# Optimization experiments

Hardware: AMD Instinct MI355X
Metric: run time of the kernel (lower is better)

The kernel has to match this reference:

```python
import jax, jax.numpy as jnp
import numpy as np


def setup_inputs() -> dict:
    key = jax.random.key(0)
    kx, kw = jax.random.split(key)
    B, C, O, H, W = 16, 32, 32, 256, 256
    x = jax.random.normal(kx, (B, C, H, W), dtype=jnp.float32)
    # Xavier-uniform init for weights of shape (O, C, H, W):
    fan_in = C * H * W
    fan_out = O * H * W
    limit = float(np.sqrt(6.0 / (fan_in + fan_out)))
    weights = jax.random.uniform(kw, (O, C, H, W), dtype=jnp.float32,
                                 minval=-limit, maxval=limit)
    return {"x": x, "weights": weights}


def reference(x, weights):
    # x: (B, C, H, W) real; weights: (O, C, H, W) real
    B, C, H, W = x.shape
    x_f = jnp.fft.rfft2(x)        # (B, C, H, W//2+1) complex
    k_f = jnp.fft.rfft2(weights)  # (O, C, H, W//2+1) complex
    # Contract channels per frequency bin instead of materializing
    # the B x O x C x H x (W//2+1) broadcast intermediate.
    out_f = jnp.einsum("bchw,ochw->bohw", x_f, k_f)
    out = jnp.fft.irfft2(out_f, s=(H, W))  # (B, O, H, W) real
    return out
```

## Files before the change

### kernel.cpp

```cpp
#include <hip/hip_runtime.h>
#include <math.h>


#define PITCH 136
#define SW(i) ((i) + ((i) >> 4))

__device__ __forceinline__ int drev4(int x) {
  int r = (int)(__brev((unsigned)x) >> 24);
  return ((r & 0x55) << 1) | ((r >> 1) & 0x55);
}

__device__ __forceinline__ void fill_tw256(float2* tw, float sign, int tid) {
  float ang = sign * 6.2831853071795864769f * (float)tid * (1.0f / 256.0f);
  float s, c;
  __sincosf(ang, &s, &c);
  tw[tid] = make_float2(c, s);
}

__device__ __forceinline__ float2 cmul(float2 a, float2 b) {
  return make_float2(fmaf(a.x, b.x, -(a.y * b.y)), fmaf(a.x, b.y, a.y * b.x));
}

template <int SIGN>
__device__ __forceinline__ void bfly4(float2 x0, float2 x1, float2 x2, float2 x3,
                                      float2 t1, float2 t2, float2 t3,
                                      float2& y0, float2& y1, float2& y2, float2& y3) {
  float2 a1 = cmul(x1, t1);
  float2 a2 = cmul(x2, t2);
  float2 a3 = cmul(x3, t3);
  float Ax = x0.x + a2.x, Ay = x0.y + a2.y;
  float Bx = x0.x - a2.x, By = x0.y - a2.y;
  float Cx = a1.x + a3.x, Cy = a1.y + a3.y;
  float Dx = a1.x - a3.x, Dy = a1.y - a3.y;
  y0 = make_float2(Ax + Cx, Ay + Cy);
  y2 = make_float2(Ax - Cx, Ay - Cy);
  if (SIGN == 1) {
    y1 = make_float2(Bx - Dy, By + Dx);
    y3 = make_float2(Bx + Dy, By - Dx);
  } else {
    y1 = make_float2(Bx + Dy, By - Dx);
    y3 = make_float2(Bx - Dy, By + Dx);
  }
}

__global__ __launch_bounds__(256) void rfft_rows(const float* __restrict__ xin,
                                                 const float* __restrict__ win,
                                                 float2* __restrict__ xout,
                                                 float2* __restrict__ wout) {
  __shared__ float2 sc[4 * 272];
  __shared__ float2 tw[256];
  const int tid = threadIdx.x;
  fill_tw256(tw, -1.f, tid);
  int blk = blockIdx.x;
  const float* in;
  float2* out;
  if (blk < 16384) {
    in = xin + (long)blk * 8 * 256;
    out = xout + (long)blk * 8 * PITCH;
  } else {
    blk -= 16384;
    in = win + (long)blk * 8 * 256;
    out = wout + (long)blk * 8 * PITCH;
  }
  const int p = tid >> 6, lt = tid & 63;
  float2* s = sc + p * 272;
  {
    int n0 = lt * 4;
    float4 v0 = *(const float4*)(in + (2 * p) * 256 + n0);
    float4 v1 = *(const float4*)(in + (2 * p + 1) * 256 + n0);
    s[SW(drev4(n0))]     = make_float2(v0.x, v1.x);
    s[SW(drev4(n0 + 1))] = make_float2(v0.y, v1.y);
    s[SW(drev4(n0 + 2))] = make_float2(v0.z, v1.z);
    s[SW(drev4(n0 + 3))] = make_float2(v0.w, v1.w);
  }
  __syncthreads();
#pragma unroll
  for (int st = 0; st < 4; ++st) {
    const int sh2 = 2 * st;
    const int L = 1 << sh2;
    const int sh = 6 - sh2;
    int j = lt & (L - 1);
    int i0 = ((lt >> sh2) << (sh2 + 2)) + j;
    float2 t1 = tw[j << sh];
    float2 t2 = tw[(2 * j) << sh];
    float2 t3 = tw[(3 * j) << sh];
    float2 x0 = s[SW(i0)], x1 = s[SW(i0 + L)];
    float2 x2 = s[SW(i0 + 2 * L)], x3 = s[SW(i0 + 3 * L)];
    float2 y0, y1, y2, y3;
    bfly4<-1>(x0, x1, x2, x3, t1, t2, t3, y0, y1, y2, y3);
    s[SW(i0)] = y0;
    s[SW(i0 + L)] = y1;
    s[SW(i0 + 2 * L)] = y2;
    s[SW(i0 + 3 * L)] = y3;
    __syncthreads();
  }
  float2* op0 = out + (2 * p) * PITCH;
  float2* op1 = out + (2 * p + 1) * PITCH;
#pragma unroll
  for (int half = 0; half < 2; ++half) {
    int k = lt + 64 * half;
    float2 U = s[SW(k)];
    float2 Vc = s[SW((256 - k) & 255)];
    float2 V = make_float2(Vc.x, -Vc.y);
    float2 A = make_float2(0.5f * (U.x + V.x), 0.5f * (U.y + V.y));
    float Wx = U.x - V.x, Wy = U.y - V.y;
    float2 Bv = make_float2(0.5f * Wy, -0.5f * Wx);
    op0[k] = A;
    op1[k] = Bv;
  }
  if (lt == 0) {
    float2 Z = s[SW(128)];
    op0[128] = make_float2(Z.x, 0.f);
    op1[128] = make_float2(Z.y, 0.f);
  }
}

template <int SIGN, int TW_>
__device__ __forceinline__ void fft_cols_body(float2* __restrict__ base,
                                              float2* __restrict__ sc,
                                              const float2* __restrict__ tw,
                                              int tid) {
  constexpr int LGT = (TW_ == 16) ? 4 : 3;
#pragma unroll
  for (int r = 0; r < TW_ / 2; ++r) {
    int f = r * 256 + tid;
    int c2 = f & (TW_ / 2 - 1);
    int h = f >> (LGT - 1);
    float4 v = *(const float4*)(base + (long)h * PITCH + c2 * 2);
    int hb = drev4(h);
    sc[hb * TW_ + c2 * 2]     = make_float2(v.x, v.y);
    sc[hb * TW_ + c2 * 2 + 1] = make_float2(v.z, v.w);
  }
  __syncthreads();
#pragma unroll
  for (int st = 0; st < 4; ++st) {
    const int sh2 = 2 * st;
    const int L = 1 << sh2;
    const int sh = 6 - sh2;
#pragma unroll
    for (int q = 0; q < TW_ / 4; ++q) {
      int e = q * 256 + tid;
      int col = e & (TW_ - 1);
      int k = e >> LGT;
      int j = k & (L - 1);
      int i0 = ((k >> sh2) << (sh2 + 2)) + j;
      float2 t1 = tw[j << sh];
      float2 t2 = tw[(2 * j) << sh];
      float2 t3 = tw[(3 * j) << sh];
      float2* p0 = &sc[i0 * TW_ + col];
      float2 x0 = p0[0], x1 = p0[L * TW_], x2 = p0[2 * L * TW_], x3 = p0[3 * L * TW_];
      float2 y0, y1, y2, y3;
      bfly4<SIGN>(x0, x1, x2, x3, t1, t2, t3, y0, y1, y2, y3);
      p0[0] = y0;
      p0[L * TW_] = y1;
      p0[2 * L * TW_] = y2;
      p0[3 * L * TW_] = y3;
    }
    __syncthreads();
  }
#pragma unroll
  for (int r = 0; r < TW_ / 2; ++r) {
    int f = r * 256 + tid;
    int c2 = f & (TW_ / 2 - 1);
    int h = f >> (LGT - 1);
    float2 a = sc[h * TW_ + c2 * 2], b = sc[h * TW_ + c2 * 2 + 1];
    *(float4*)(base + (long)h * PITCH + c2 * 2) = make_float4(a.x, a.y, b.x, b.y);
  }
}

template <int SIGN>
__global__ __launch_bounds__(256) void fft_cols(float2* __restrict__ data) {
  __shared__ float2 sc[256 * 16];
  __shared__ float2 tw[256];
  const int tid = threadIdx.x;
  fill_tw256(tw, (float)SIGN, tid);
  if (blockIdx.y < 8) {
    float2* base = data + (long)blockIdx.x * 256 * PITCH + blockIdx.y * 16;
    fft_cols_body<SIGN, 16>(base, sc, tw, tid);
  } else {
    float2* base = data + (long)blockIdx.x * 256 * PITCH + 128;
    fft_cols_body<SIGN, 8>(base, sc, tw, tid);
  }
}

__global__ __launch_bounds__(256, 3) void einsum_kernel(float2* __restrict__ xf,
                                                        const float2* __restrict__ wf) {
  __shared__ __align__(16) float2 Xs[8 * 256];
  __shared__ __align__(16) float2 Ws[8 * 32 * 16];
  const int h = blockIdx.x;
  const int tid = threadIdx.x;

  if (blockIdx.y == 8) {
    const long off = (long)h * PITCH + 128;
    for (int e = tid; e < 512; e += 256)  Xs[e] = xf[(long)e * 256 * PITCH + off];
    for (int e = tid; e < 1024; e += 256) Ws[e] = wf[(long)e * 256 * PITCH + off];
    __syncthreads();
    const int b = tid >> 4, o0 = (tid & 15) * 2;
    float2 a0 = make_float2(0.f, 0.f), a1 = make_float2(0.f, 0.f);
#pragma unroll
    for (int c = 0; c < 32; ++c) {
      float2 x = Xs[b * 32 + c];
      float2 w0 = Ws[o0 * 32 + c];
      float2 w1 = Ws[(o0 + 1) * 32 + c];
      a0.x = fmaf(x.x, w0.x, fmaf(-x.y, w0.y, a0.x));
      a0.y = fmaf(x.x, w0.y, fmaf(x.y, w0.x, a0.y));
      a1.x = fmaf(x.x, w1.x, fmaf(-x.y, w1.y, a1.x));
      a1.y = fmaf(x.x, w1.y, fmaf(x.y, w1.x, a1.y));
    }
    xf[(long)(b * 32 + o0) * 256 * PITCH + off] = a0;
    xf[(long)(b * 32 + o0 + 1) * 256 * PITCH + off] = a1;
    return;
  }

  const int wb = tid & 15, b = tid >> 4;
  const long hoff = (long)h * PITCH + blockIdx.y * 16;
  float2 acc[32];
#pragma unroll
  for (int o = 0; o < 32; ++o) acc[o] = make_float2(0.f, 0.f);

  const float2* gX[4];
  float2* sX[4];
#pragma unroll
  for (int r = 0; r < 4; ++r) {
    int e = r * 256 + tid, lw = e & 7, lc = (e >> 3) & 7, lb = e >> 6;
    gX[r] = xf + (long)(lb * 32 + lc) * 256 * PITCH + hoff + lw * 2;
    sX[r] = &Xs[lc * 256 + lb * 16 + lw * 2];
  }
  const float2* gW[8];
  float2* sW[8];
#pragma unroll
  for (int r = 0; r < 8; ++r) {
    int e = r * 256 + tid, lw = e & 7, lc = (e >> 3) & 7, lo = e >> 6;
    gW[r] = wf + (long)(lo * 32 + lc) * 256 * PITCH + hoff + lw * 2;
    sW[r] = &Ws[(lc * 32 + lo) * 16 + lw * 2];
  }
  const long cstep = (long)8 * 256 * PITCH;

  float4 px[4], pw[8];
#pragma unroll
  for (int r = 0; r < 4; ++r) px[r] = *(const float4*)gX[r];
#pragma unroll
  for (int r = 0; r < 8; ++r) pw[r] = *(const float4*)gW[r];

  for (int c0 = 0; c0 < 32; c0 += 8) {
#pragma unroll
    for (int r = 0; r < 4; ++r) *(float4*)sX[r] = px[r];
#pragma unroll
    for (int r = 0; r < 8; ++r) *(float4*)sW[r] = pw[r];
    __syncthreads();
    if (c0 < 24) {
#pragma unroll
      for (int r = 0; r < 4; ++r) { gX[r] += cstep; px[r] = *(const float4*)gX[r]; }
#pragma unroll
      for (int r = 0; r < 8; ++r) { gW[r] += cstep; pw[r] = *(const float4*)gW[r]; }
    }
#pragma unroll
    for (int c = 0; c < 8; ++c) {
      float2 xv = Xs[c * 256 + tid];
#pragma unroll
      for (int o = 0; o < 32; ++o) {
        float2 wv = Ws[(c * 32 + o) * 16 + wb];
        acc[o].x = fmaf(xv.x, wv.x, fmaf(-xv.y, wv.y, acc[o].x));
        acc[o].y = fmaf(xv.x, wv.y, fmaf(xv.y, wv.x, acc[o].y));
      }
    }
    __syncthreads();
  }
#pragma unroll
  for (int o = 0; o < 32; ++o)
    xf[(long)(b * 32 + o) * 256 * PITCH + hoff + wb] = acc[o];
}

__global__ __launch_bounds__(256) void irfft_rows(const float2* __restrict__ in,
                                                  float* __restrict__ out) {
  __shared__ float2 sc[4 * 272];
  __shared__ float2 tw[256];
  const int tid = threadIdx.x;
  fill_tw256(tw, 1.f, tid);
  const long row0 = (long)blockIdx.x * 8;
  const int p = tid >> 6, lt = tid & 63;
  float2* s = sc + p * 272;
  const float2* ip0 = in + (row0 + 2 * p) * PITCH;
  const float2* ip1 = in + (row0 + 2 * p + 1) * PITCH;
#pragma unroll
  for (int q = 0; q < 4; ++q) {
    int k = lt + 64 * q;
    int m = (k <= 128) ? k : 256 - k;
    float2 U0 = ip0[m], U1 = ip1[m];
    float2 z;
    if (k <= 128) z = make_float2(U0.x - U1.y, U0.y + U1.x);
    else          z = make_float2(U0.x + U1.y, U1.x - U0.y);
    s[SW(drev4(k))] = z;
  }
  __syncthreads();
#pragma unroll
  for (int st = 0; st < 4; ++st) {
    const int sh2 = 2 * st;
    const int L = 1 << sh2;
    const int sh = 6 - sh2;
    int j = lt & (L - 1);
    int i0 = ((lt >> sh2) << (sh2 + 2)) + j;
    float2 t1 = tw[j << sh];
    float2 t2 = tw[(2 * j) << sh];
    float2 t3 = tw[(3 * j) << sh];
    float2 x0 = s[SW(i0)], x1 = s[SW(i0 + L)];
    float2 x2 = s[SW(i0 + 2 * L)], x3 = s[SW(i0 + 3 * L)];
    float2 y0, y1, y2, y3;
    bfly4<1>(x0, x1, x2, x3, t1, t2, t3, y0, y1, y2, y3);
    s[SW(i0)] = y0;
    s[SW(i0 + L)] = y1;
    s[SW(i0 + 2 * L)] = y2;
    s[SW(i0 + 3 * L)] = y3;
    __syncthreads();
  }
  const float scale = 1.f / 65536.f;
  float* o0 = out + (row0 + 2 * p) * 256;
  float* o1 = out + (row0 + 2 * p + 1) * 256;
  int n0 = lt * 4;
  float2 e0 = s[SW(n0)], e1 = s[SW(n0 + 1)], e2 = s[SW(n0 + 2)], e3 = s[SW(n0 + 3)];
  *(float4*)(o0 + n0) = make_float4(e0.x * scale, e1.x * scale, e2.x * scale, e3.x * scale);
  *(float4*)(o1 + n0) = make_float4(e0.y * scale, e1.y * scale, e2.y * scale, e3.y * scale);
}

extern "C" void kernel_launch(void* const* d_in, const int* in_sizes, int n_in,
                              void* d_out, int out_size, void* d_ws, size_t ws_size,
                              hipStream_t stream) {
  const float* x = (const float*)d_in[0];
  const float* w = (const float*)d_in[1];
  float* out = (float*)d_out;

  const size_t row_elems = (size_t)256 * PITCH;
  const size_t need = (size_t)(512 + 1024) * row_elems * sizeof(float2);
  if (ws_size < need) return;

  float2* Xf = (float2*)d_ws;
  float2* Wf = Xf + (size_t)512 * row_elems;

  rfft_rows<<<dim3(16384 + 32768), 256, 0, stream>>>(x, w, Xf, Wf);
  fft_cols<-1><<<dim3(1536, 9), 256, 0, stream>>>(Xf);
  einsum_kernel<<<dim3(256, 9), 256, 0, stream>>>(Xf, Wf);
  fft_cols<1><<<dim3(512, 9), 256, 0, stream>>>(Xf);
  irfft_rows<<<dim3(16384), 256, 0, stream>>>(Xf, out);
}
```

Baseline: 1.085 ms.

## Use register radix-16 four-step FFT for column transforms; drop einsum register prefetch

Column FFTs on 16-wide tiles switch from four shared-memory radix-4 stages with a barrier after each to a 16x16 four-step decomposition done in registers: a DFT16, a twiddle multiply, a transpose through shared memory, and a second DFT16. This removes the bit-reversal load and most of the shared-memory round trips and barriers. The einsum kernel separately drops its register double-buffered global prefetch in favour of direct load-then-store into shared memory, which frees registers but exposes load latency. A barrier is added after the twiddle table fill.

```diff
diff --git a/kernel.cpp b/kernel.cpp
--- a/kernel.cpp
+++ b/kernel.cpp
@@ -43,6 +43,33 @@
   }
 }
 
+template <int SIGN>
+__device__ __forceinline__ void dft16(float2 v[16]) {
+  const float C1 = 0.92387953251128675613f;
+  const float S1 = 0.38268343236508977173f;
+  const float R2 = 0.70710678118654752440f;
+  const float s = (float)SIGN;
+  const float2 ONE = make_float2(1.f, 0.f);
+  const float2 W1 = make_float2(C1, s * S1);
+  const float2 W2 = make_float2(R2, s * R2);
+  const float2 W3 = make_float2(S1, s * C1);
+  const float2 W4 = make_float2(0.f, s);
+  const float2 W6 = make_float2(-R2, s * R2);
+  const float2 W9 = make_float2(-C1, -s * S1);
+  float2 t[4][4];
+#pragma unroll
+  for (int b = 0; b < 4; ++b)
+    bfly4<SIGN>(v[b], v[b + 4], v[b + 8], v[b + 12], ONE, ONE, ONE,
+                t[b][0], t[b][1], t[b][2], t[b][3]);
+  t[1][1] = cmul(t[1][1], W1); t[1][2] = cmul(t[1][2], W2); t[1][3] = cmul(t[1][3], W3);
+  t[2][1] = cmul(t[2][1], W2); t[2][2] = cmul(t[2][2], W4); t[2][3] = cmul(t[2][3], W6);
+  t[3][1] = cmul(t[3][1], W3); t[3][2] = cmul(t[3][2], W6); t[3][3] = cmul(t[3][3], W9);
+#pragma unroll
+  for (int k1 = 0; k1 < 4; ++k1)
+    bfly4<SIGN>(t[0][k1], t[1][k1], t[2][k1], t[3][k1], ONE, ONE, ONE,
+                v[k1], v[k1 + 4], v[k1 + 8], v[k1 + 12]);
+}
+
 __global__ __launch_bounds__(256) void rfft_rows(const float* __restrict__ xin,
                                                  const float* __restrict__ win,
                                                  float2* __restrict__ xout,
@@ -115,12 +142,56 @@
   }
 }
 
-template <int SIGN, int TW_>
-__device__ __forceinline__ void fft_cols_body(float2* __restrict__ base,
-                                              float2* __restrict__ sc,
-                                              const float2* __restrict__ tw,
-                                              int tid) {
-  constexpr int LGT = (TW_ == 16) ? 4 : 3;
+template <int SIGN>
+__device__ __forceinline__ void fft_cols_body16(float2* __restrict__ base,
+                                                float2* __restrict__ sc,
+                                                const float2* __restrict__ tw,
+                                                int tid) {
+#pragma unroll
+  for (int r = 0; r < 8; ++r) {
+    int f = r * 256 + tid;
+    int c2 = f & 7;
+    int h = f >> 3;
+    float4 v = *(const float4*)(base + (long)h * PITCH + c2 * 2);
+    sc[h * 16 + c2 * 2]     = make_float2(v.x, v.y);
+    sc[h * 16 + c2 * 2 + 1] = make_float2(v.z, v.w);
+  }
+  __syncthreads();
+  const int wb = tid & 15, n1 = tid >> 4;
+  float2 xr[16];
+#pragma unroll
+  for (int n2 = 0; n2 < 16; ++n2) xr[n2] = sc[(16 * n2 + n1) * 16 + wb];
+  dft16<SIGN>(xr);
+#pragma unroll
+  for (int K = 1; K < 16; ++K) xr[K] = cmul(xr[K], tw[n1 * K]);
+  __syncthreads();
+#pragma unroll
+  for (int K = 0; K < 16; ++K) sc[(n1 * 16 + K) * 16 + wb] = xr[K];
+  __syncthreads();
+  const int k1 = tid >> 4;
+  float2 zr[16];
+#pragma unroll
+  for (int m = 0; m < 16; ++m) zr[m] = sc[(m * 16 + k1) * 16 + wb];
+  dft16<SIGN>(zr);
+#pragma unroll
+  for (int k2 = 0; k2 < 16; ++k2) sc[(k1 + 16 * k2) * 16 + wb] = zr[k2];
+  __syncthreads();
+#pragma unroll
+  for (int r = 0; r < 8; ++r) {
+    int f = r * 256 + tid;
+    int c2 = f & 7;
+    int h = f >> 3;
+    float2 a = sc[h * 16 + c2 * 2], b = sc[h * 16 + c2 * 2 + 1];
+    *(float4*)(base + (long)h * PITCH + c2 * 2) = make_float4(a.x, a.y, b.x, b.y);
+  }
+}
+
+template <int SIGN>
+__device__ __forceinline__ void fft_cols_body8(float2* __restrict__ base,
+                                               float2* __restrict__ sc,
+                                               const float2* __restrict__ tw,
+                                               int tid) {
+  constexpr int TW_ = 8, LGT = 3;
 #pragma unroll
   for (int r = 0; r < TW_ / 2; ++r) {
     int f = r * 256 + tid;
@@ -174,19 +245,20 @@
   __shared__ float2 tw[256];
   const int tid = threadIdx.x;
   fill_tw256(tw, (float)SIGN, tid);
+  __syncthreads();
   if (blockIdx.y < 8) {
     float2* base = data + (long)blockIdx.x * 256 * PITCH + blockIdx.y * 16;
-    fft_cols_body<SIGN, 16>(base, sc, tw, tid);
+    fft_cols_body16<SIGN>(base, sc, tw, tid);
   } else {
     float2* base = data + (long)blockIdx.x * 256 * PITCH + 128;
-    fft_cols_body<SIGN, 8>(base, sc, tw, tid);
+    fft_cols_body8<SIGN>(base, sc, tw, tid);
   }
 }
 
 __global__ __launch_bounds__(256, 3) void einsum_kernel(float2* __restrict__ xf,
                                                         const float2* __restrict__ wf) {
-  __shared__ __align__(16) float2 Xs[8 * 256];
-  __shared__ __align__(16) float2 Ws[8 * 32 * 16];
+  __shared__ float2 Xs[8 * 256];
+  __shared__ float2 Ws[8 * 32 * 16];
   const int h = blockIdx.x;
   const int tid = threadIdx.x;
 
@@ -218,42 +290,24 @@
 #pragma unroll
   for (int o = 0; o < 32; ++o) acc[o] = make_float2(0.f, 0.f);
 
-  const float2* gX[4];
-  float2* sX[4];
-#pragma unroll
-  for (int r = 0; r < 4; ++r) {
-    int e = r * 256 + tid, lw = e & 7, lc = (e >> 3) & 7, lb = e >> 6;
-    gX[r] = xf + (long)(lb * 32 + lc) * 256 * PITCH + hoff + lw * 2;
-    sX[r] = &Xs[lc * 256 + lb * 16 + lw * 2];
-  }
-  const float2* gW[8];
-  float2* sW[8];
-#pragma unroll
-  for (int r = 0; r < 8; ++r) {
-    int e = r * 256 + tid, lw = e & 7, lc = (e >> 3) & 7, lo = e >> 6;
-    gW[r] = wf + (long)(lo * 32 + lc) * 256 * PITCH + hoff + lw * 2;
-    sW[r] = &Ws[(lc * 32 + lo) * 16 + lw * 2];
-  }
-  const long cstep = (long)8 * 256 * PITCH;
-
-  float4 px[4], pw[8];
-#pragma unroll
-  for (int r = 0; r < 4; ++r) px[r] = *(const float4*)gX[r];
-#pragma unroll
-  for (int r = 0; r < 8; ++r) pw[r] = *(const float4*)gW[r];
-
   for (int c0 = 0; c0 < 32; c0 += 8) {
 #pragma unroll
-    for (int r = 0; r < 4; ++r) *(float4*)sX[r] = px[r];
-#pragma unroll
-    for (int r = 0; r < 8; ++r) *(float4*)sW[r] = pw[r];
-    __syncthreads();
-    if (c0 < 24) {
-#pragma unroll
-      for (int r = 0; r < 4; ++r) { gX[r] += cstep; px[r] = *(const float4*)gX[r]; }
-#pragma unroll
-      for (int r = 0; r < 8; ++r) { gW[r] += cstep; pw[r] = *(const float4*)gW[r]; }
-    }
+    for (int r = 0; r < 4; ++r) {
+      int e = r * 256 + tid;
+      int lw = e & 7, lc = (e >> 3) & 7, lb = e >> 6;
+      float4 v = *(const float4*)(xf + (long)(lb * 32 + c0 + lc) * 256 * PITCH + hoff + lw * 2);
+      Xs[lc * 256 + lb * 16 + lw * 2]     = make_float2(v.x, v.y);
+      Xs[lc * 256 + lb * 16 + lw * 2 + 1] = make_float2(v.z, v.w);
+    }
+#pragma unroll
+    for (int r = 0; r < 8; ++r) {
+      int e = r * 256 + tid;
+      int lw = e & 7, lc = (e >> 3) & 7, lo = e >> 6;
+      float4 v = *(const float4*)(wf + (long)(lo * 32 + c0 + lc) * 256 * PITCH + hoff + lw * 2);
+      Ws[(lc * 32 + lo) * 16 + lw * 2]     = make_float2(v.x, v.y);
+      Ws[(lc * 32 + lo) * 16 + lw * 2 + 1] = make_float2(v.z, v.w);
+    }
+    __syncthreads();
 #pragma unroll
     for (int c = 0; c < 8; ++c) {
       float2 xv = Xs[c * 256 + tid];
```

After: 1.039 ms. 4.2% less time.
